# Kernel optimization log

Hardware: AMD Instinct MI355X
Metric: run time of the kernel (lower is better)

## Reference

```python
import jax, jax.numpy as jnp
import numpy as np

B = 262144
L = 16      # latent_dim
H = 64      # hidden_dim
C = 8       # num_charts
O = 32      # output_dim
TAU_MIN = 0.01
TAU_DENOM_MIN = 0.001
EPS = 0.001
LN_EPS = 1e-5


def setup_inputs() -> dict:
    key = jax.random.key(0)
    ks = jax.random.split(key, 16)
    # latents kept well inside the Poincare ball
    z_geo = 0.1 * jax.random.normal(ks[0], (B, L), dtype=jnp.float32)
    z_tex = 0.1 * jax.random.normal(ks[1], (B, L), dtype=jnp.float32)
    def lin(k, fan_in, shape):
        bound = 1.0 / np.sqrt(fan_in)
        return jax.random.uniform(k, shape, jnp.float32, -bound, bound)
    chart_w = lin(ks[2], L, (C, H, L))   # stacked per-chart Linear weights
    chart_b = lin(ks[3], L, (C, H))
    router_w = lin(ks[4], L, (C, L))
    router_b = lin(ks[5], L, (C,))
    centers = 0.02 * jax.random.normal(ks[6], (C, L), dtype=jnp.float32)
    tex_w = lin(ks[7], L, (H, L))
    tex_b = lin(ks[8], L, (H,))
    ln_g = jnp.ones((H,), jnp.float32)
    ln_b = jnp.zeros((H,), jnp.float32)
    w1 = lin(ks[9], H, (H, H))
    b1 = lin(ks[10], H, (H,))
    w2 = lin(ks[11], H, (O, H))
    b2 = lin(ks[12], H, (O,))
    return dict(z_geo=z_geo, z_tex=z_tex, chart_w=chart_w, chart_b=chart_b,
                router_w=router_w, router_b=router_b, centers=centers,
                tex_w=tex_w, tex_b=tex_b, ln_g=ln_g, ln_b=ln_b,
                w1=w1, b1=b1, w2=w2, b2=b2)


def _temperature(z):
    r2 = jnp.sum(z * z, axis=-1)                      # [B]
    denom = jnp.maximum(1.0 - r2, TAU_DENOM_MIN)
    tau = (np.sqrt(L) * denom) * 0.5
    return jnp.maximum(tau, TAU_MIN)                  # [B]


def _gelu(x):
    return jax.nn.gelu(x, approximate=False)


def reference(z_geo, z_tex, chart_w, chart_b, router_w, router_b, centers,
              tex_w, tex_b, ln_g, ln_b, w1, b1, w2, b2):
    # hyperbolic distance scores  [B, C]
    diff = z_geo[:, None, :] - centers[None, :, :]
    dist_sq = jnp.sum(diff * diff, axis=-1)
    z_sq = jnp.sum(z_geo * z_geo, axis=-1, keepdims=True)   # [B,1]
    c_sq = jnp.sum(centers * centers, axis=-1)[None, :]      # [1,C]
    denom = (1.0 - z_sq) * (1.0 - c_sq)
    arg = 1.0 + 2.0 * dist_sq / (denom + EPS)
    dist = jnp.arccosh(jnp.maximum(arg, 1.0 + EPS))
    tau = _temperature(z_geo)                                # [B]
    scores = -dist / tau[:, None]
    scores = scores + 0.1 * (z_geo @ router_w.T + router_b) / tau[:, None]
    router_weights = jax.nn.softmax(scores, axis=-1)         # [B,C]

    # dense chart projection + weighted blend
    h_stack = jnp.einsum('bl,chl->bch', z_geo, chart_w) + chart_b[None]  # [B,C,H]
    h_global = jnp.sum(h_stack * router_weights[:, :, None], axis=1)     # [B,H]
    h_tex = z_tex @ tex_w.T + tex_b
    h = h_global + h_tex

    # renderer: LayerNorm -> GELU -> Linear -> GELU -> Linear
    mu = jnp.mean(h, axis=-1, keepdims=True)
    var = jnp.mean((h - mu) ** 2, axis=-1, keepdims=True)
    hn = (h - mu) * jax.lax.rsqrt(var + LN_EPS) * ln_g + ln_b
    h1 = _gelu(_gelu(hn) @ w1.T + b1)
    x_hat = h1 @ w2.T + b2
    return x_hat, router_weights
```

## Files before the change

### kernel.cpp

```cpp
#include <hip/hip_runtime.h>
#include <hip/hip_bf16.h>
#include <hip/hip_fp16.h>


typedef __attribute__((ext_vector_type(8))) short short8;
typedef __attribute__((ext_vector_type(4))) float f32x4;

__device__ __forceinline__ int pkbf2(float a, float b) {
    union { __hip_bfloat162 h2; int i; } u;
    u.h2 = __float22bfloat162_rn(make_float2(a, b));
    return u.i;
}
__device__ __forceinline__ short pkbf1(float a) { return (short)pkbf2(a, 0.f); }

__device__ __forceinline__ float gelu_fast(float x) {
    float x2 = x * x;
    float t  = __expf(fmaf(x2, 0.07135481f, 1.5957691f) * x);
    float r  = __builtin_amdgcn_rcpf(t + 1.0f);
    return fmaf(-x, r, x);
}
__device__ __forceinline__ int bpack(int k, int n, int KT) {
    return (((n >> 4) * KT + (k >> 5)) * 64 + (n & 15) + (((k & 31) >> 3) << 4)) * 8 + (k & 7);
}
__device__ __forceinline__ int gswz(int g) {
    return g ^ (((g >> 4) & 3) << 1) ^ ((g >> 3) & 1);
}
__device__ __forceinline__ short8 packrow8(const float* base) {
    const float4* p = (const float4*)base;
    float4 a = p[0], b = p[1];
    union { short8 s; int i[4]; } f;
    f.i[0] = pkbf2(a.x, a.y); f.i[1] = pkbf2(a.z, a.w);
    f.i[2] = pkbf2(b.x, b.y); f.i[3] = pkbf2(b.z, b.w);
    return f.s;
}

__global__ void pack_weights(const float* __restrict__ cw, const float* __restrict__ cb,
                             const float* __restrict__ txw, const float* __restrict__ txb,
                             const float* __restrict__ w1,  const float* __restrict__ w2,
                             short* __restrict__ ws)
{
    const int tid = threadIdx.x;
    for (int idx = tid; idx < 160 * 64; idx += 256) {
        int k = idx >> 6, n = idx & 63;
        float v;
        if (k < 128)       v = cw[(k >> 4) * 1024 + n * 16 + (k & 15)];
        else if (k < 144)  v = txw[n * 16 + (k - 128)];
        else if (k < 152)  v = cb[(k - 144) * 64 + n];
        else if (k == 152) v = txb[n];
        else               v = 0.f;
        ws[bpack(k, n, 5)] = pkbf1(v);
    }
    for (int f = tid; f < 512; f += 256) {
        int lane = f & 63, e = f >> 6;
        int nt = e >> 1, kt = e & 1;
        int col = lane & 15, qq = lane >> 4;
        *(short8*)(ws + 10240 + f * 8) = packrow8(w1 + (nt * 16 + col) * 64 + kt * 32 + qq * 8);
    }
    {
        int f = tid;
        int lane = f & 63, e = f >> 6;
        int nt = e >> 1, kt = e & 1;
        int col = lane & 15, qq = lane >> 4;
        *(short8*)(ws + 14336 + f * 8) = packrow8(w2 + (nt * 16 + col) * 64 + kt * 32 + qq * 8);
    }
}

constexpr int SCR_OFF = 20480;
constexpr int RS_OFF  = 28672;
constexpr int SMEM_SZ = 32768;

__global__ __launch_bounds__(256, 4) void topo_mfma(
    const float* __restrict__ zg,  const float* __restrict__ ztx,
    const float* __restrict__ cw,  const float* __restrict__ cb,
    const float* __restrict__ rw,  const float* __restrict__ rb,
    const float* __restrict__ cen, const float* __restrict__ txw,
    const float* __restrict__ txb, const float* __restrict__ lng,
    const float* __restrict__ lnb, const float* __restrict__ w1,
    const float* __restrict__ b1,  const float* __restrict__ w2,
    const float* __restrict__ b2,  const short* __restrict__ wsp,
    const int prepacked,
    float* __restrict__ out, int Btot)
{
    __shared__ __align__(16) char smem[SMEM_SZ];
    short* WA = (short*)smem;
    __half* RSh = (__half*)(smem + RS_OFF);

    const int tid = threadIdx.x;
    const int wv = tid >> 6, lane = tid & 63;
    const int q = lane >> 4, col = lane & 15;
    const int sub = (lane >> 3) & 1, j = lane & 7;

    if (prepacked) {
        const int4* src = (const int4*)wsp;
        int4* dst = (int4*)smem;
        #pragma unroll
        for (int i = 0; i < 5; i++) dst[i * 256 + tid] = src[i * 256 + tid];
    } else {
        for (int idx = tid; idx < 160 * 64; idx += 256) {
            int k = idx >> 6, n = idx & 63;
            float v;
            if (k < 128)       v = cw[(k >> 4) * 1024 + n * 16 + (k & 15)];
            else if (k < 144)  v = txw[n * 16 + (k - 128)];
            else if (k < 152)  v = cb[(k - 144) * 64 + n];
            else if (k == 152) v = txb[n];
            else               v = 0.f;
            WA[bpack(k, n, 5)] = pkbf1(v);
        }
    }

    const long sG = (long)blockIdx.x * 256 + tid;
    {
        float z[16];
        const float4* pg = (const float4*)(zg + sG * 16);
        #pragma unroll
        for (int v = 0; v < 4; v++) {
            float4 a = pg[v];
            z[v*4+0]=a.x; z[v*4+1]=a.y; z[v*4+2]=a.z; z[v*4+3]=a.w;
        }
        float r2 = 0.f;
        #pragma unroll
        for (int l = 0; l < 16; l++) r2 = fmaf(z[l], z[l], r2);
        const float inv_tau = __builtin_amdgcn_rcpf(fmaxf(2.0f * fmaxf(1.0f - r2, 0.001f), 0.01f));
        const float omr2 = 1.0f - r2;
        float scv[8]; float smax = -1e30f;
        #pragma unroll
        for (int c = 0; c < 8; c++) {
            const float4* cp = (const float4*)(cen + c * 16);
            const float4* rp = (const float4*)(rw  + c * 16);
            float dsq = 0.f, csq = 0.f, dotv = 0.f;
            #pragma unroll
            for (int v = 0; v < 4; v++) {
                float4 cv = cp[v], rv = rp[v];
                float d0 = z[v*4+0] - cv.x, d1 = z[v*4+1] - cv.y;
                float d2 = z[v*4+2] - cv.z, d3 = z[v*4+3] - cv.w;
                dsq  = fmaf(d0,d0, fmaf(d1,d1, fmaf(d2,d2, fmaf(d3,d3, dsq))));
                csq  = fmaf(cv.x,cv.x, fmaf(cv.y,cv.y, fmaf(cv.z,cv.z, fmaf(cv.w,cv.w, csq))));
                dotv = fmaf(z[v*4+0],rv.x, fmaf(z[v*4+1],rv.y,
                       fmaf(z[v*4+2],rv.z, fmaf(z[v*4+3],rv.w, dotv))));
            }
            float u = 2.0f * dsq * __builtin_amdgcn_rcpf(omr2 * (1.0f - csq) + 0.001f);
            u = fmaxf(u, 0.001f);
            float dist  = __logf((1.0f + u) + __builtin_amdgcn_sqrtf(u * (u + 2.0f)));
            float score = fmaf(0.1f, dotv + rb[c], -dist) * inv_tau;
            scv[c] = score; smax = fmaxf(smax, score);
        }
        float esum = 0.f;
        #pragma unroll
        for (int c = 0; c < 8; c++) { scv[c] = __expf(scv[c] - smax); esum += scv[c]; }
        const float rinv = __builtin_amdgcn_rcpf(esum);
        union { ushort us[8]; int4 v; } hv;
        #pragma unroll
        for (int c = 0; c < 8; c++) {
            scv[c] *= rinv;
            hv.us[(c & 1) * 4 + (c >> 1)] = __half_as_ushort(__float2half_rn(scv[c]));
        }
        *(int4*)(RSh + tid * 8) = hv.v;
        float4* pr = (float4*)(out + (long)Btot * 32 + sG * 8);
        pr[0] = make_float4(scv[0], scv[1], scv[2], scv[3]);
        pr[1] = make_float4(scv[4], scv[5], scv[6], scv[7]);
    }

    short8 W1F[4][2], W2F[2][2];
    if (prepacked) {
        const short8* p1 = (const short8*)(wsp + 10240);
        #pragma unroll
        for (int nt = 0; nt < 4; nt++)
            #pragma unroll
            for (int kt = 0; kt < 2; kt++)
                W1F[nt][kt] = p1[(nt * 2 + kt) * 64 + lane];
        const short8* p2 = (const short8*)(wsp + 14336);
        #pragma unroll
        for (int nt = 0; nt < 2; nt++)
            #pragma unroll
            for (int kt = 0; kt < 2; kt++)
                W2F[nt][kt] = p2[(nt * 2 + kt) * 64 + lane];
    } else {
        const int kb = q * 8;
        #pragma unroll
        for (int nt = 0; nt < 4; nt++)
            #pragma unroll
            for (int kt = 0; kt < 2; kt++)
                W1F[nt][kt] = packrow8(w1 + (nt * 16 + col) * 64 + kt * 32 + kb);
        #pragma unroll
        for (int nt = 0; nt < 2; nt++)
            #pragma unroll
            for (int kt = 0; kt < 2; kt++)
                W2F[nt][kt] = packrow8(w2 + (nt * 16 + col) * 64 + kt * 32 + kb);
    }

    float lngv[4], lnbv[4], b1v[4], b2v[2];
    #pragma unroll
    for (int nt = 0; nt < 4; nt++) {
        lngv[nt] = lng[nt * 16 + col];
        lnbv[nt] = lnb[nt * 16 + col];
        b1v[nt]  = b1[nt * 16 + col];
    }
    b2v[0] = b2[col]; b2v[1] = b2[16 + col];

    __syncthreads();

    short* scr = (short*)(smem + SCR_OFF) + wv * 1024;
    union Frag { short8 s; int i[4]; };

    const long blockBase = (long)blockIdx.x * 256;
    const float* zrow = zg  + (blockBase + wv * 64 + col) * 16 + ((q & 1) << 3);
    const float* trow = ztx + (blockBase + wv * 64 + col) * 16 + ((q & 1) << 3);

    float4 za = ((const float4*)zrow)[0], zb = ((const float4*)zrow)[1];
    float4 ta = ((const float4*)trow)[0], tb = ((const float4*)trow)[1];

    for (int t = 0; t < 4; t++) {
        const int mBase = wv * 64 + t * 16;
        const int sL = mBase + col;
        const int rsb = sL * 8;

        float rc[4];
        {
            union { unsigned long long u; __half2 h[2]; } rr;
            rr.u = *(const unsigned long long*)(RSh + rsb + ((q >> 1) << 2));
            float2 f0 = __half22float2(rr.h[0]);
            float2 f1 = __half22float2(rr.h[1]);
            rc[0] = f0.x; rc[1] = f0.y; rc[2] = f1.x; rc[3] = f1.y;
        }

        f32x4 acc[4] = {{0.f,0.f,0.f,0.f},{0.f,0.f,0.f,0.f},{0.f,0.f,0.f,0.f},{0.f,0.f,0.f,0.f}};
        #pragma unroll
        for (int kt = 0; kt < 4; kt++) {
            float r = rc[kt];
            Frag f;
            f.i[0] = pkbf2(r * za.x, r * za.y);
            f.i[1] = pkbf2(r * za.z, r * za.w);
            f.i[2] = pkbf2(r * zb.x, r * zb.y);
            f.i[3] = pkbf2(r * zb.z, r * zb.w);
            #pragma unroll
            for (int nt = 0; nt < 4; nt++) {
                short8 bf = *(const short8*)(WA + (nt * 5 + kt) * 512 + lane * 8);
                acc[nt] = __builtin_amdgcn_mfma_f32_16x16x32_bf16(f.s, bf, acc[nt], 0, 0, 0);
            }
        }
        {
            Frag f;
            if (q < 2) {
                f.i[0] = pkbf2(ta.x, ta.y); f.i[1] = pkbf2(ta.z, ta.w);
                f.i[2] = pkbf2(tb.x, tb.y); f.i[3] = pkbf2(tb.z, tb.w);
            } else if (q == 2) {
                union { int4 u; __half2 h[4]; } rv;
                rv.u = *(const int4*)(RSh + rsb);
                float2 e0 = __half22float2(rv.h[0]);
                float2 e1 = __half22float2(rv.h[1]);
                float2 e2 = __half22float2(rv.h[2]);
                float2 e3 = __half22float2(rv.h[3]);
                f.i[0] = pkbf2(e0.x, e2.x);
                f.i[1] = pkbf2(e0.y, e2.y);
                f.i[2] = pkbf2(e1.x, e3.x);
                f.i[3] = pkbf2(e1.y, e3.y);
            } else {
                f.i[0] = pkbf2(1.0f, 0.f); f.i[1] = 0; f.i[2] = 0; f.i[3] = 0;
            }
            #pragma unroll
            for (int nt = 0; nt < 4; nt++) {
                short8 bf = *(const short8*)(WA + (nt * 5 + 4) * 512 + lane * 8);
                acc[nt] = __builtin_amdgcn_mfma_f32_16x16x32_bf16(f.s, bf, acc[nt], 0, 0, 0);
            }
        }

        if (t < 3) {
            const float4* pzn = (const float4*)(zrow + (t + 1) * 256);
            const float4* ptn = (const float4*)(trow + (t + 1) * 256);
            za = pzn[0]; zb = pzn[1]; ta = ptn[0]; tb = ptn[1];
        }

        float mu[4], rsd[4];
        #pragma unroll
        for (int reg = 0; reg < 4; reg++) {
            float a = acc[0][reg], b = acc[1][reg], c = acc[2][reg], d = acc[3][reg];
            float s  = (a + b) + (c + d);
            float s2 = fmaf(a, a, fmaf(b, b, fmaf(c, c, d * d)));
            s  += __shfl_xor(s, 1);  s  += __shfl_xor(s, 2);
            s  += __shfl_xor(s, 4);  s  += __shfl_xor(s, 8);
            s2 += __shfl_xor(s2, 1); s2 += __shfl_xor(s2, 2);
            s2 += __shfl_xor(s2, 4); s2 += __shfl_xor(s2, 8);
            float m = s * (1.0f / 64.0f);
            mu[reg]  = m;
            rsd[reg] = rsqrtf(fmaf(s2, 1.0f / 64.0f, -m * m) + 1e-5f);
        }

        #pragma unroll
        for (int nt = 0; nt < 4; nt++) {
            int high = (nt & 1) * 2 + sub;
            #pragma unroll
            for (int reg = 0; reg < 4; reg++) {
                float hn = (acc[nt][reg] - mu[reg]) * rsd[reg] * lngv[nt] + lnbv[nt];
                int grp = gswz((q * 4 + reg) + 16 * high);
                scr[(nt >> 1) * 512 + grp * 8 + j] = pkbf1(gelu_fast(hn));
            }
        }
        asm volatile("s_waitcnt lgkmcnt(0)" ::: "memory");

        short8 A2[2];
        {
            int grp = gswz(lane);
            A2[0] = *(const short8*)(scr +       grp * 8);
            A2[1] = *(const short8*)(scr + 512 + grp * 8);
        }

        #pragma unroll
        for (int nt = 0; nt < 4; nt++) {
            f32x4 a2 = {0.f, 0.f, 0.f, 0.f};
            a2 = __builtin_amdgcn_mfma_f32_16x16x32_bf16(A2[0], W1F[nt][0], a2, 0, 0, 0);
            a2 = __builtin_amdgcn_mfma_f32_16x16x32_bf16(A2[1], W1F[nt][1], a2, 0, 0, 0);
            int high = (nt & 1) * 2 + sub;
            #pragma unroll
            for (int reg = 0; reg < 4; reg++) {
                float h1v = gelu_fast(a2[reg] + b1v[nt]);
                int grp = gswz((q * 4 + reg) + 16 * high);
                scr[(nt >> 1) * 512 + grp * 8 + j] = pkbf1(h1v);
            }
        }
        asm volatile("s_waitcnt lgkmcnt(0)" ::: "memory");

        short8 A3[2];
        {
            int grp = gswz(lane);
            A3[0] = *(const short8*)(scr +       grp * 8);
            A3[1] = *(const short8*)(scr + 512 + grp * 8);
        }

        const long sOutBase = blockBase + mBase + q * 4;
        #pragma unroll
        for (int nt = 0; nt < 2; nt++) {
            f32x4 a3 = {0.f, 0.f, 0.f, 0.f};
            a3 = __builtin_amdgcn_mfma_f32_16x16x32_bf16(A3[0], W2F[nt][0], a3, 0, 0, 0);
            a3 = __builtin_amdgcn_mfma_f32_16x16x32_bf16(A3[1], W2F[nt][1], a3, 0, 0, 0);
            #pragma unroll
            for (int reg = 0; reg < 4; reg++)
                out[(sOutBase + reg) * 32 + nt * 16 + col] = a3[reg] + b2v[nt];
        }
    }
}

extern "C" void kernel_launch(void* const* d_in, const int* in_sizes, int n_in,
                              void* d_out, int out_size, void* d_ws, size_t ws_size,
                              hipStream_t stream) {
    const int B = in_sizes[0] / 16;
    const int prepacked = (d_ws != nullptr && ws_size >= 32768) ? 1 : 0;
    if (prepacked) {
        hipLaunchKernelGGL(pack_weights, dim3(1), dim3(256), 0, stream,
            (const float*)d_in[2],  (const float*)d_in[3],
            (const float*)d_in[7],  (const float*)d_in[8],
            (const float*)d_in[11], (const float*)d_in[13],
            (short*)d_ws);
    }
    dim3 grid(B / 256), block(256);
    hipLaunchKernelGGL(topo_mfma, grid, block, 0, stream,
        (const float*)d_in[0],  (const float*)d_in[1],
        (const float*)d_in[2],  (const float*)d_in[3],
        (const float*)d_in[4],  (const float*)d_in[5],
        (const float*)d_in[6],  (const float*)d_in[7],
        (const float*)d_in[8],  (const float*)d_in[9],
        (const float*)d_in[10], (const float*)d_in[11],
        (const float*)d_in[12], (const float*)d_in[13],
        (const float*)d_in[14],
        (const short*)d_ws, prepacked,
        (float*)d_out, B);
}
```

Measured before the change: 147.6 us.

## Transpose MFMA operands so activations chain through registers via lane shuffles

New measurement: 221.5 us. +50.1%, slower.

```diff
diff --git a/kernel.cpp b/kernel.cpp
--- a/kernel.cpp
+++ b/kernel.cpp
@@ -18,12 +18,6 @@
     float t  = __expf(fmaf(x2, 0.07135481f, 1.5957691f) * x);
     float r  = __builtin_amdgcn_rcpf(t + 1.0f);
     return fmaf(-x, r, x);
-}
-__device__ __forceinline__ int bpack(int k, int n, int KT) {
-    return (((n >> 4) * KT + (k >> 5)) * 64 + (n & 15) + (((k & 31) >> 3) << 4)) * 8 + (k & 7);
-}
-__device__ __forceinline__ int gswz(int g) {
-    return g ^ (((g >> 4) & 3) << 1) ^ ((g >> 3) & 1);
 }
 __device__ __forceinline__ short8 packrow8(const float* base) {
     const float4* p = (const float4*)base;
@@ -34,40 +28,73 @@
     return f.s;
 }
 
+__device__ __forceinline__ void bfly(int (&D)[4][2], bool hi32, bool hi16) {
+    #pragma unroll
+    for (int n1 = 0; n1 < 2; n1++)
+        #pragma unroll
+        for (int s = 0; s < 2; s++) {
+            int d0 = D[n1*2+0][s], d1 = D[n1*2+1][s];
+            int send = hi32 ? d0 : d1;
+            int recv = __shfl_xor(send, 32);
+            D[n1*2+0][s] = hi32 ? recv : d0;
+            D[n1*2+1][s] = hi32 ? d1 : recv;
+        }
+    #pragma unroll
+    for (int n1 = 0; n1 < 2; n1++)
+        #pragma unroll
+        for (int s = 0; s < 2; s++) {
+            int d0 = D[n1*2+0][s], d1 = D[n1*2+1][s];
+            int send = hi16 ? d0 : d1;
+            int recv = __shfl_xor(send, 16);
+            D[n1*2+0][s] = hi16 ? recv : d0;
+            D[n1*2+1][s] = hi16 ? d1 : recv;
+        }
+}
+
 __global__ void pack_weights(const float* __restrict__ cw, const float* __restrict__ cb,
                              const float* __restrict__ txw, const float* __restrict__ txb,
                              const float* __restrict__ w1,  const float* __restrict__ w2,
+                             const float* __restrict__ cen, const float* __restrict__ rb,
                              short* __restrict__ ws)
 {
     const int tid = threadIdx.x;
-    for (int idx = tid; idx < 160 * 64; idx += 256) {
-        int k = idx >> 6, n = idx & 63;
+    for (int idx = tid; idx < 10240; idx += 256) {
+        int j = idx & 7, lane = (idx >> 3) & 63, g = idx >> 9;
+        int nt = g / 5, kt = g - nt * 5;
+        int k = kt * 32 + (lane >> 4) * 8 + j;
+        int n = nt * 16 + (lane & 15);
         float v;
         if (k < 128)       v = cw[(k >> 4) * 1024 + n * 16 + (k & 15)];
         else if (k < 144)  v = txw[n * 16 + (k - 128)];
         else if (k < 152)  v = cb[(k - 144) * 64 + n];
         else if (k == 152) v = txb[n];
         else               v = 0.f;
-        ws[bpack(k, n, 5)] = pkbf1(v);
-    }
-    for (int f = tid; f < 512; f += 256) {
+        ws[idx] = pkbf1(v);
+    }
+    for (int f = tid; f < 768; f += 256) {
         int lane = f & 63, e = f >> 6;
-        int nt = e >> 1, kt = e & 1;
         int col = lane & 15, qq = lane >> 4;
-        *(short8*)(ws + 10240 + f * 8) = packrow8(w1 + (nt * 16 + col) * 64 + kt * 32 + qq * 8);
-    }
-    {
-        int f = tid;
-        int lane = f & 63, e = f >> 6;
-        int nt = e >> 1, kt = e & 1;
-        int col = lane & 15, qq = lane >> 4;
-        *(short8*)(ws + 14336 + f * 8) = packrow8(w2 + (nt * 16 + col) * 64 + kt * 32 + qq * 8);
-    }
-}
-
-constexpr int SCR_OFF = 20480;
-constexpr int RS_OFF  = 28672;
-constexpr int SMEM_SZ = 32768;
+        if (e < 8) {
+            int nt = e >> 1, kt = e & 1;
+            *(short8*)(ws + 10240 + f * 8) =
+                packrow8(w1 + (nt * 16 + col) * 64 + kt * 32 + qq * 8);
+        } else {
+            int e2 = e - 8, nt = e2 >> 1, kt = e2 & 1;
+            *(short8*)(ws + 14336 + (e2 * 64 + lane) * 8) =
+                packrow8(w2 + (nt * 16 + col) * 64 + kt * 32 + qq * 8);
+        }
+    }
+    if (tid < 8) {
+        float csq = 0.f;
+        for (int l = 0; l < 16; l++) { float cv = cen[tid * 16 + l]; csq = fmaf(cv, cv, csq); }
+        ((float4*)((char*)ws + 32768))[tid] = make_float4(csq, 1.0f - csq, 0.1f * rb[tid], 0.f);
+    }
+}
+
+constexpr int W1L_OFF = 20480;
+constexpr int W2L_OFF = 28672;
+constexpr int RS_OFF  = 32768;
+constexpr int SMEM_SZ = 36864;
 
 __global__ __launch_bounds__(256, 4) void topo_mfma(
     const float* __restrict__ zg,  const float* __restrict__ ztx,
@@ -82,29 +109,47 @@
     float* __restrict__ out, int Btot)
 {
     __shared__ __align__(16) char smem[SMEM_SZ];
-    short* WA = (short*)smem;
+    short* WAF = (short*)smem;
+    const short8* W1L = (const short8*)(smem + W1L_OFF);
+    const short8* W2L = (const short8*)(smem + W2L_OFF);
     __half* RSh = (__half*)(smem + RS_OFF);
 
     const int tid = threadIdx.x;
     const int wv = tid >> 6, lane = tid & 63;
     const int q = lane >> 4, col = lane & 15;
-    const int sub = (lane >> 3) & 1, j = lane & 7;
+    const bool hi32 = (lane & 32) != 0, hi16 = (lane & 16) != 0;
 
     if (prepacked) {
         const int4* src = (const int4*)wsp;
         int4* dst = (int4*)smem;
         #pragma unroll
-        for (int i = 0; i < 5; i++) dst[i * 256 + tid] = src[i * 256 + tid];
+        for (int i = 0; i < 8; i++) dst[i * 256 + tid] = src[i * 256 + tid];
     } else {
-        for (int idx = tid; idx < 160 * 64; idx += 256) {
-            int k = idx >> 6, n = idx & 63;
+        for (int idx = tid; idx < 10240; idx += 256) {
+            int j = idx & 7, ln = (idx >> 3) & 63, g = idx >> 9;
+            int nt = g / 5, kt = g - nt * 5;
+            int k = kt * 32 + (ln >> 4) * 8 + j;
+            int n = nt * 16 + (ln & 15);
             float v;
             if (k < 128)       v = cw[(k >> 4) * 1024 + n * 16 + (k & 15)];
             else if (k < 144)  v = txw[n * 16 + (k - 128)];
             else if (k < 152)  v = cb[(k - 144) * 64 + n];
             else if (k == 152) v = txb[n];
             else               v = 0.f;
-            WA[bpack(k, n, 5)] = pkbf1(v);
+            WAF[idx] = pkbf1(v);
+        }
+        for (int f = tid; f < 768; f += 256) {
+            int ln = f & 63, e = f >> 6;
+            int c_ = ln & 15, qq = ln >> 4;
+            if (e < 8) {
+                int nt = e >> 1, kt = e & 1;
+                *(short8*)(smem + W1L_OFF + f * 16) =
+                    packrow8(w1 + (nt * 16 + c_) * 64 + kt * 32 + qq * 8);
+            } else {
+                int e2 = e - 8, nt = e2 >> 1, kt = e2 & 1;
+                *(short8*)(smem + W2L_OFF + (e2 * 64 + ln) * 16) =
+                    packrow8(w2 + (nt * 16 + c_) * 64 + kt * 32 + qq * 8);
+            }
         }
     }
 
@@ -122,26 +167,35 @@
         for (int l = 0; l < 16; l++) r2 = fmaf(z[l], z[l], r2);
         const float inv_tau = __builtin_amdgcn_rcpf(fmaxf(2.0f * fmaxf(1.0f - r2, 0.001f), 0.01f));
         const float omr2 = 1.0f - r2;
+        const float4* cvp = (const float4*)((const char*)wsp + 32768);
         float scv[8]; float smax = -1e30f;
         #pragma unroll
         for (int c = 0; c < 8; c++) {
+            float csq, omc2, rb1;
+            if (prepacked) {
+                float4 kv = cvp[c]; csq = kv.x; omc2 = kv.y; rb1 = kv.z;
+            } else {
+                csq = 0.f;
+                #pragma unroll
+                for (int l = 0; l < 16; l++) { float cv = cen[c*16+l]; csq = fmaf(cv, cv, csq); }
+                omc2 = 1.0f - csq; rb1 = 0.1f * rb[c];
+            }
             const float4* cp = (const float4*)(cen + c * 16);
             const float4* rp = (const float4*)(rw  + c * 16);
-            float dsq = 0.f, csq = 0.f, dotv = 0.f;
+            float zc = 0.f, dotv = 0.f;
             #pragma unroll
             for (int v = 0; v < 4; v++) {
                 float4 cv = cp[v], rv = rp[v];
-                float d0 = z[v*4+0] - cv.x, d1 = z[v*4+1] - cv.y;
-                float d2 = z[v*4+2] - cv.z, d3 = z[v*4+3] - cv.w;
-                dsq  = fmaf(d0,d0, fmaf(d1,d1, fmaf(d2,d2, fmaf(d3,d3, dsq))));
-                csq  = fmaf(cv.x,cv.x, fmaf(cv.y,cv.y, fmaf(cv.z,cv.z, fmaf(cv.w,cv.w, csq))));
+                zc   = fmaf(z[v*4+0],cv.x, fmaf(z[v*4+1],cv.y,
+                       fmaf(z[v*4+2],cv.z, fmaf(z[v*4+3],cv.w, zc))));
                 dotv = fmaf(z[v*4+0],rv.x, fmaf(z[v*4+1],rv.y,
                        fmaf(z[v*4+2],rv.z, fmaf(z[v*4+3],rv.w, dotv))));
             }
-            float u = 2.0f * dsq * __builtin_amdgcn_rcpf(omr2 * (1.0f - csq) + 0.001f);
+            float dsq = fmaf(-2.0f, zc, r2 + csq);
+            float u = 2.0f * dsq * __builtin_amdgcn_rcpf(omr2 * omc2 + 0.001f);
             u = fmaxf(u, 0.001f);
             float dist  = __logf((1.0f + u) + __builtin_amdgcn_sqrtf(u * (u + 2.0f)));
-            float score = fmaf(0.1f, dotv + rb[c], -dist) * inv_tau;
+            float score = (fmaf(0.1f, dotv, rb1) - dist) * inv_tau;
             scv[c] = score; smax = fmaxf(smax, score);
         }
         float esum = 0.f;
@@ -160,47 +214,21 @@
         pr[1] = make_float4(scv[4], scv[5], scv[6], scv[7]);
     }
 
-    short8 W1F[4][2], W2F[2][2];
-    if (prepacked) {
-        const short8* p1 = (const short8*)(wsp + 10240);
-        #pragma unroll
-        for (int nt = 0; nt < 4; nt++)
-            #pragma unroll
-            for (int kt = 0; kt < 2; kt++)
-                W1F[nt][kt] = p1[(nt * 2 + kt) * 64 + lane];
-        const short8* p2 = (const short8*)(wsp + 14336);
-        #pragma unroll
-        for (int nt = 0; nt < 2; nt++)
-            #pragma unroll
-            for (int kt = 0; kt < 2; kt++)
-                W2F[nt][kt] = p2[(nt * 2 + kt) * 64 + lane];
-    } else {
-        const int kb = q * 8;
-        #pragma unroll
-        for (int nt = 0; nt < 4; nt++)
-            #pragma unroll
-            for (int kt = 0; kt < 2; kt++)
-                W1F[nt][kt] = packrow8(w1 + (nt * 16 + col) * 64 + kt * 32 + kb);
-        #pragma unroll
-        for (int nt = 0; nt < 2; nt++)
-            #pragma unroll
-            for (int kt = 0; kt < 2; kt++)
-                W2F[nt][kt] = packrow8(w2 + (nt * 16 + col) * 64 + kt * 32 + kb);
-    }
-
-    float lngv[4], lnbv[4], b1v[4], b2v[2];
+    float lngv[4][4], lnbv[4][4], b1v[4][4], b2v[2];
     #pragma unroll
     for (int nt = 0; nt < 4; nt++) {
-        lngv[nt] = lng[nt * 16 + col];
-        lnbv[nt] = lnb[nt * 16 + col];
-        b1v[nt]  = b1[nt * 16 + col];
+        float4 g4 = *(const float4*)(lng + nt * 16 + q * 4);
+        float4 bb = *(const float4*)(lnb + nt * 16 + q * 4);
+        float4 o4 = *(const float4*)(b1  + nt * 16 + q * 4);
+        lngv[nt][0]=g4.x; lngv[nt][1]=g4.y; lngv[nt][2]=g4.z; lngv[nt][3]=g4.w;
+        lnbv[nt][0]=bb.x; lnbv[nt][1]=bb.y; lnbv[nt][2]=bb.z; lnbv[nt][3]=bb.w;
+        b1v [nt][0]=o4.x; b1v [nt][1]=o4.y; b1v [nt][2]=o4.z; b1v [nt][3]=o4.w;
     }
     b2v[0] = b2[col]; b2v[1] = b2[16 + col];
 
     __syncthreads();
 
-    short* scr = (short*)(smem + SCR_OFF) + wv * 1024;
-    union Frag { short8 s; int i[4]; };
+    union FragU { short8 s; int i[4]; };
 
     const long blockBase = (long)blockIdx.x * 256;
     const float* zrow = zg  + (blockBase + wv * 64 + col) * 16 + ((q & 1) << 3);
@@ -227,19 +255,19 @@
         #pragma unroll
         for (int kt = 0; kt < 4; kt++) {
             float r = rc[kt];
-            Frag f;
+            FragU f;
             f.i[0] = pkbf2(r * za.x, r * za.y);
             f.i[1] = pkbf2(r * za.z, r * za.w);
             f.i[2] = pkbf2(r * zb.x, r * zb.y);
             f.i[3] = pkbf2(r * zb.z, r * zb.w);
             #pragma unroll
             for (int nt = 0; nt < 4; nt++) {
-                short8 bf = *(const short8*)(WA + (nt * 5 + kt) * 512 + lane * 8);
-                acc[nt] = __builtin_amdgcn_mfma_f32_16x16x32_bf16(f.s, bf, acc[nt], 0, 0, 0);
+                short8 wa = *(const short8*)(WAF + ((nt * 5 + kt) * 64 + lane) * 8);
+                acc[nt] = __builtin_amdgcn_mfma_f32_16x16x32_bf16(wa, f.s, acc[nt], 0, 0, 0);
             }
         }
         {
-            Frag f;
+            FragU f;
             if (q < 2) {
                 f.i[0] = pkbf2(ta.x, ta.y); f.i[1] = pkbf2(ta.z, ta.w);
                 f.i[2] = pkbf2(tb.x, tb.y); f.i[3] = pkbf2(tb.z, tb.w);
@@ -259,8 +287,8 @@
             }
             #pragma unroll
             for (int nt = 0; nt < 4; nt++) {
-                short8 bf = *(const short8*)(WA + (nt * 5 + 4) * 512 + lane * 8);
-                acc[nt] = __builtin_amdgcn_mfma_f32_16x16x32_bf16(f.s, bf, acc[nt], 0, 0, 0);
+                short8 wa = *(const short8*)(WAF + ((nt * 5 + 4) * 64 + lane) * 8);
+                acc[nt] = __builtin_amdgcn_mfma_f32_16x16x32_bf16(wa, f.s, acc[nt], 0, 0, 0);
             }
         }
 
@@ -270,68 +298,61 @@
             za = pzn[0]; zb = pzn[1]; ta = ptn[0]; tb = ptn[1];
         }
 
-        float mu[4], rsd[4];
-        #pragma unroll
-        for (int reg = 0; reg < 4; reg++) {
-            float a = acc[0][reg], b = acc[1][reg], c = acc[2][reg], d = acc[3][reg];
-            float s  = (a + b) + (c + d);
-            float s2 = fmaf(a, a, fmaf(b, b, fmaf(c, c, d * d)));
-            s  += __shfl_xor(s, 1);  s  += __shfl_xor(s, 2);
-            s  += __shfl_xor(s, 4);  s  += __shfl_xor(s, 8);
-            s2 += __shfl_xor(s2, 1); s2 += __shfl_xor(s2, 2);
-            s2 += __shfl_xor(s2, 4); s2 += __shfl_xor(s2, 8);
-            float m = s * (1.0f / 64.0f);
-            mu[reg]  = m;
-            rsd[reg] = rsqrtf(fmaf(s2, 1.0f / 64.0f, -m * m) + 1e-5f);
-        }
-
-        #pragma unroll
-        for (int nt = 0; nt < 4; nt++) {
-            int high = (nt & 1) * 2 + sub;
+        float s = 0.f, s2 = 0.f;
+        #pragma unroll
+        for (int nt = 0; nt < 4; nt++)
             #pragma unroll
             for (int reg = 0; reg < 4; reg++) {
-                float hn = (acc[nt][reg] - mu[reg]) * rsd[reg] * lngv[nt] + lnbv[nt];
-                int grp = gswz((q * 4 + reg) + 16 * high);
-                scr[(nt >> 1) * 512 + grp * 8 + j] = pkbf1(gelu_fast(hn));
-            }
-        }
-        asm volatile("s_waitcnt lgkmcnt(0)" ::: "memory");
-
-        short8 A2[2];
-        {
-            int grp = gswz(lane);
-            A2[0] = *(const short8*)(scr +       grp * 8);
-            A2[1] = *(const short8*)(scr + 512 + grp * 8);
-        }
-
+                float v = acc[nt][reg];
+                s += v; s2 = fmaf(v, v, s2);
+            }
+        s  += __shfl_xor(s, 16);  s  += __shfl_xor(s, 32);
+        s2 += __shfl_xor(s2, 16); s2 += __shfl_xor(s2, 32);
+        float mu  = s * (1.0f / 64.0f);
+        float rsd = rsqrtf(fmaf(s2, 1.0f / 64.0f, -mu * mu) + 1e-5f);
+
+        int D[4][2];
+        #pragma unroll
+        for (int nt = 0; nt < 4; nt++)
+            #pragma unroll
+            for (int sx = 0; sx < 2; sx++) {
+                float g0 = gelu_fast(fmaf((acc[nt][2*sx  ] - mu) * rsd, lngv[nt][2*sx  ], lnbv[nt][2*sx  ]));
+                float g1 = gelu_fast(fmaf((acc[nt][2*sx+1] - mu) * rsd, lngv[nt][2*sx+1], lnbv[nt][2*sx+1]));
+                D[nt][sx] = pkbf2(g0, g1);
+            }
+        bfly(D, hi32, hi16);
+        FragU Gf0, Gf1;
+        Gf0.i[0]=D[0][0]; Gf0.i[1]=D[0][1]; Gf0.i[2]=D[1][0]; Gf0.i[3]=D[1][1];
+        Gf1.i[0]=D[2][0]; Gf1.i[1]=D[2][1]; Gf1.i[2]=D[3][0]; Gf1.i[3]=D[3][1];
+
+        int D2[4][2];
         #pragma unroll
         for (int nt = 0; nt < 4; nt++) {
             f32x4 a2 = {0.f, 0.f, 0.f, 0.f};
-            a2 = __builtin_amdgcn_mfma_f32_16x16x32_bf16(A2[0], W1F[nt][0], a2, 0, 0, 0);
-            a2 = __builtin_amdgcn_mfma_f32_16x16x32_bf16(A2[1], W1F[nt][1], a2, 0, 0, 0);
-            int high = (nt & 1) * 2 + sub;
-            #pragma unroll
-            for (int reg = 0; reg < 4; reg++) {
-                float h1v = gelu_fast(a2[reg] + b1v[nt]);
-                int grp = gswz((q * 4 + reg) + 16 * high);
-                scr[(nt >> 1) * 512 + grp * 8 + j] = pkbf1(h1v);
-            }
-        }
-        asm volatile("s_waitcnt lgkmcnt(0)" ::: "memory");
-
-        short8 A3[2];
-        {
-            int grp = gswz(lane);
-            A3[0] = *(const short8*)(scr +       grp * 8);
-            A3[1] = *(const short8*)(scr + 512 + grp * 8);
-        }
+            short8 wA = W1L[(nt * 2 + 0) * 64 + lane];
+            short8 wB = W1L[(nt * 2 + 1) * 64 + lane];
+            a2 = __builtin_amdgcn_mfma_f32_16x16x32_bf16(wA, Gf0.s, a2, 0, 0, 0);
+            a2 = __builtin_amdgcn_mfma_f32_16x16x32_bf16(wB, Gf1.s, a2, 0, 0, 0);
+            #pragma unroll
+            for (int sx = 0; sx < 2; sx++) {
+                float h0 = gelu_fast(a2[2*sx  ] + b1v[nt][2*sx  ]);
+                float h1 = gelu_fast(a2[2*sx+1] + b1v[nt][2*sx+1]);
+                D2[nt][sx] = pkbf2(h0, h1);
+            }
+        }
+        bfly(D2, hi32, hi16);
+        FragU A3f0, A3f1;
+        A3f0.i[0]=D2[0][0]; A3f0.i[1]=D2[0][1]; A3f0.i[2]=D2[1][0]; A3f0.i[3]=D2[1][1];
+        A3f1.i[0]=D2[2][0]; A3f1.i[1]=D2[2][1]; A3f1.i[2]=D2[3][0]; A3f1.i[3]=D2[3][1];
 
         const long sOutBase = blockBase + mBase + q * 4;
         #pragma unroll
         for (int nt = 0; nt < 2; nt++) {
             f32x4 a3 = {0.f, 0.f, 0.f, 0.f};
-            a3 = __builtin_amdgcn_mfma_f32_16x16x32_bf16(A3[0], W2F[nt][0], a3, 0, 0, 0);
-            a3 = __builtin_amdgcn_mfma_f32_16x16x32_bf16(A3[1], W2F[nt][1], a3, 0, 0, 0);
+            short8 wA = W2L[(nt * 2 + 0) * 64 + lane];
+            short8 wB = W2L[(nt * 2 + 1) * 64 + lane];
+            a3 = __builtin_amdgcn_mfma_f32_16x16x32_bf16(A3f0.s, wA, a3, 0, 0, 0);
+            a3 = __builtin_amdgcn_mfma_f32_16x16x32_bf16(A3f1.s, wB, a3, 0, 0, 0);
             #pragma unroll
             for (int reg = 0; reg < 4; reg++)
                 out[(sOutBase + reg) * 32 + nt * 16 + col] = a3[reg] + b2v[nt];
@@ -343,12 +364,13 @@
                               void* d_out, int out_size, void* d_ws, size_t ws_size,
                               hipStream_t stream) {
     const int B = in_sizes[0] / 16;
-    const int prepacked = (d_ws != nullptr && ws_size >= 32768) ? 1 : 0;
+    const int prepacked = (d_ws != nullptr && ws_size >= 32896) ? 1 : 0;
     if (prepacked) {
         hipLaunchKernelGGL(pack_weights, dim3(1), dim3(256), 0, stream,
             (const float*)d_in[2],  (const float*)d_in[3],
             (const float*)d_in[7],  (const float*)d_in[8],
             (const float*)d_in[11], (const float*)d_in[13],
+            (const float*)d_in[6],  (const float*)d_in[5],
             (short*)d_ws);
     }
     dim3 grid(B / 256), block(256);
```

## Move W2 fragments to LDS, precompute center norms, restructure first MFMA loop

Applied to the files above, without the earlier changes.

New measurement: 151.9 us. 1.03x slower.

```diff
diff --git a/kernel.cpp b/kernel.cpp
--- a/kernel.cpp
+++ b/kernel.cpp
@@ -37,6 +37,7 @@
 __global__ void pack_weights(const float* __restrict__ cw, const float* __restrict__ cb,
                              const float* __restrict__ txw, const float* __restrict__ txb,
                              const float* __restrict__ w1,  const float* __restrict__ w2,
+                             const float* __restrict__ cen, const float* __restrict__ rb,
                              short* __restrict__ ws)
 {
     const int tid = threadIdx.x;
@@ -63,11 +64,17 @@
         int col = lane & 15, qq = lane >> 4;
         *(short8*)(ws + 14336 + f * 8) = packrow8(w2 + (nt * 16 + col) * 64 + kt * 32 + qq * 8);
     }
+    if (tid < 8) {
+        float csq = 0.f;
+        for (int l = 0; l < 16; l++) { float cv = cen[tid * 16 + l]; csq = fmaf(cv, cv, csq); }
+        ((float4*)((char*)ws + 32768))[tid] = make_float4(csq, 1.0f - csq, 0.1f * rb[tid], 0.f);
+    }
 }
 
 constexpr int SCR_OFF = 20480;
 constexpr int RS_OFF  = 28672;
-constexpr int SMEM_SZ = 32768;
+constexpr int W2L_OFF = 32768;
+constexpr int SMEM_SZ = 36864;
 
 __global__ __launch_bounds__(256, 4) void topo_mfma(
     const float* __restrict__ zg,  const float* __restrict__ ztx,
@@ -84,6 +91,7 @@
     __shared__ __align__(16) char smem[SMEM_SZ];
     short* WA = (short*)smem;
     __half* RSh = (__half*)(smem + RS_OFF);
+    const short8* W2L = (const short8*)(smem + W2L_OFF);
 
     const int tid = threadIdx.x;
     const int wv = tid >> 6, lane = tid & 63;
@@ -95,6 +103,7 @@
         int4* dst = (int4*)smem;
         #pragma unroll
         for (int i = 0; i < 5; i++) dst[i * 256 + tid] = src[i * 256 + tid];
+        ((int4*)(smem + W2L_OFF))[tid] = ((const int4*)((const char*)wsp + 28672))[tid];
     } else {
         for (int idx = tid; idx < 160 * 64; idx += 256) {
             int k = idx >> 6, n = idx & 63;
@@ -106,6 +115,12 @@
             else               v = 0.f;
             WA[bpack(k, n, 5)] = pkbf1(v);
         }
+        {
+            int e = tid >> 6, ln = tid & 63;
+            int nt = e >> 1, kt = e & 1;
+            *(short8*)(smem + W2L_OFF + (e * 64 + ln) * 16) =
+                packrow8(w2 + (nt * 16 + (ln & 15)) * 64 + kt * 32 + (ln >> 4) * 8);
+        }
     }
 
     const long sG = (long)blockIdx.x * 256 + tid;
@@ -122,26 +137,35 @@
         for (int l = 0; l < 16; l++) r2 = fmaf(z[l], z[l], r2);
         const float inv_tau = __builtin_amdgcn_rcpf(fmaxf(2.0f * fmaxf(1.0f - r2, 0.001f), 0.01f));
         const float omr2 = 1.0f - r2;
+        const float4* cvp = (const float4*)((const char*)wsp + 32768);
         float scv[8]; float smax = -1e30f;
         #pragma unroll
         for (int c = 0; c < 8; c++) {
+            float csq, omc2, rb1;
+            if (prepacked) {
+                float4 kv = cvp[c]; csq = kv.x; omc2 = kv.y; rb1 = kv.z;
+            } else {
+                csq = 0.f;
+                #pragma unroll
+                for (int l = 0; l < 16; l++) { float cv = cen[c*16+l]; csq = fmaf(cv, cv, csq); }
+                omc2 = 1.0f - csq; rb1 = 0.1f * rb[c];
+            }
             const float4* cp = (const float4*)(cen + c * 16);
             const float4* rp = (const float4*)(rw  + c * 16);
-            float dsq = 0.f, csq = 0.f, dotv = 0.f;
+            float zc = 0.f, dotv = 0.f;
             #pragma unroll
             for (int v = 0; v < 4; v++) {
                 float4 cv = cp[v], rv = rp[v];
-                float d0 = z[v*4+0] - cv.x, d1 = z[v*4+1] - cv.y;
-                float d2 = z[v*4+2] - cv.z, d3 = z[v*4+3] - cv.w;
-                dsq  = fmaf(d0,d0, fmaf(d1,d1, fmaf(d2,d2, fmaf(d3,d3, dsq))));
-                csq  = fmaf(cv.x,cv.x, fmaf(cv.y,cv.y, fmaf(cv.z,cv.z, fmaf(cv.w,cv.w, csq))));
+                zc   = fmaf(z[v*4+0],cv.x, fmaf(z[v*4+1],cv.y,
+                       fmaf(z[v*4+2],cv.z, fmaf(z[v*4+3],cv.w, zc))));
                 dotv = fmaf(z[v*4+0],rv.x, fmaf(z[v*4+1],rv.y,
                        fmaf(z[v*4+2],rv.z, fmaf(z[v*4+3],rv.w, dotv))));
             }
-            float u = 2.0f * dsq * __builtin_amdgcn_rcpf(omr2 * (1.0f - csq) + 0.001f);
+            float dsq = fmaf(-2.0f, zc, r2 + csq);
+            float u = 2.0f * dsq * __builtin_amdgcn_rcpf(omr2 * omc2 + 0.001f);
             u = fmaxf(u, 0.001f);
             float dist  = __logf((1.0f + u) + __builtin_amdgcn_sqrtf(u * (u + 2.0f)));
-            float score = fmaf(0.1f, dotv + rb[c], -dist) * inv_tau;
+            float score = (fmaf(0.1f, dotv, rb1) - dist) * inv_tau;
             scv[c] = score; smax = fmaxf(smax, score);
         }
         float esum = 0.f;
@@ -160,7 +184,7 @@
         pr[1] = make_float4(scv[4], scv[5], scv[6], scv[7]);
     }
 
-    short8 W1F[4][2], W2F[2][2];
+    short8 W1F[4][2];
     if (prepacked) {
         const short8* p1 = (const short8*)(wsp + 10240);
         #pragma unroll
@@ -168,12 +192,6 @@
             #pragma unroll
             for (int kt = 0; kt < 2; kt++)
                 W1F[nt][kt] = p1[(nt * 2 + kt) * 64 + lane];
-        const short8* p2 = (const short8*)(wsp + 14336);
-        #pragma unroll
-        for (int nt = 0; nt < 2; nt++)
-            #pragma unroll
-            for (int kt = 0; kt < 2; kt++)
-                W2F[nt][kt] = p2[(nt * 2 + kt) * 64 + lane];
     } else {
         const int kb = q * 8;
         #pragma unroll
@@ -181,13 +199,7 @@
             #pragma unroll
             for (int kt = 0; kt < 2; kt++)
                 W1F[nt][kt] = packrow8(w1 + (nt * 16 + col) * 64 + kt * 32 + kb);
-        #pragma unroll
-        for (int nt = 0; nt < 2; nt++)
-            #pragma unroll
-            for (int kt = 0; kt < 2; kt++)
-                W2F[nt][kt] = packrow8(w2 + (nt * 16 + col) * 64 + kt * 32 + kb);
-    }
-
+    }
     float lngv[4], lnbv[4], b1v[4], b2v[2];
     #pragma unroll
     for (int nt = 0; nt < 4; nt++) {
@@ -210,9 +222,9 @@
     float4 ta = ((const float4*)trow)[0], tb = ((const float4*)trow)[1];
 
     for (int t = 0; t < 4; t++) {
-        const int mBase = wv * 64 + t * 16;
-        const int sL = mBase + col;
-        const int rsb = sL * 8;
+        const int  mBase = wv * 64 + t * 16;
+        const int  sL = mBase + col;
+        const int  rsb = sL * 8;
 
         float rc[4];
         {
@@ -223,7 +235,7 @@
             rc[0] = f0.x; rc[1] = f0.y; rc[2] = f1.x; rc[3] = f1.y;
         }
 
-        f32x4 acc[4] = {{0.f,0.f,0.f,0.f},{0.f,0.f,0.f,0.f},{0.f,0.f,0.f,0.f},{0.f,0.f,0.f,0.f}};
+        short8 A1[5];
         #pragma unroll
         for (int kt = 0; kt < 4; kt++) {
             float r = rc[kt];
@@ -232,11 +244,7 @@
             f.i[1] = pkbf2(r * za.z, r * za.w);
             f.i[2] = pkbf2(r * zb.x, r * zb.y);
             f.i[3] = pkbf2(r * zb.z, r * zb.w);
-            #pragma unroll
-            for (int nt = 0; nt < 4; nt++) {
-                short8 bf = *(const short8*)(WA + (nt * 5 + kt) * 512 + lane * 8);
-                acc[nt] = __builtin_amdgcn_mfma_f32_16x16x32_bf16(f.s, bf, acc[nt], 0, 0, 0);
-            }
+            A1[kt] = f.s;
         }
         {
             Frag f;
@@ -257,11 +265,20 @@
             } else {
                 f.i[0] = pkbf2(1.0f, 0.f); f.i[1] = 0; f.i[2] = 0; f.i[3] = 0;
             }
-            #pragma unroll
-            for (int nt = 0; nt < 4; nt++) {
-                short8 bf = *(const short8*)(WA + (nt * 5 + 4) * 512 + lane * 8);
-                acc[nt] = __builtin_amdgcn_mfma_f32_16x16x32_bf16(f.s, bf, acc[nt], 0, 0, 0);
-            }
+            A1[4] = f.s;
+        }
+
+        float h[4][4];
+        #pragma unroll
+        for (int nt = 0; nt < 4; nt++) {
+            f32x4 acc = {0.f, 0.f, 0.f, 0.f};
+            #pragma unroll
+            for (int kt = 0; kt < 5; kt++) {
+                short8 bf = *(const short8*)(WA + (nt * 5 + kt) * 512 + lane * 8);
+                acc = __builtin_amdgcn_mfma_f32_16x16x32_bf16(A1[kt], bf, acc, 0, 0, 0);
+            }
+            #pragma unroll
+            for (int reg = 0; reg < 4; reg++) h[nt][reg] = acc[reg];
         }
 
         if (t < 3) {
@@ -273,7 +290,7 @@
         float mu[4], rsd[4];
         #pragma unroll
         for (int reg = 0; reg < 4; reg++) {
-            float a = acc[0][reg], b = acc[1][reg], c = acc[2][reg], d = acc[3][reg];
+            float a = h[0][reg], b = h[1][reg], c = h[2][reg], d = h[3][reg];
             float s  = (a + b) + (c + d);
             float s2 = fmaf(a, a, fmaf(b, b, fmaf(c, c, d * d)));
             s  += __shfl_xor(s, 1);  s  += __shfl_xor(s, 2);
@@ -290,7 +307,7 @@
             int high = (nt & 1) * 2 + sub;
             #pragma unroll
             for (int reg = 0; reg < 4; reg++) {
-                float hn = (acc[nt][reg] - mu[reg]) * rsd[reg] * lngv[nt] + lnbv[nt];
+                float hn = (h[nt][reg] - mu[reg]) * rsd[reg] * lngv[nt] + lnbv[nt];
                 int grp = gswz((q * 4 + reg) + 16 * high);
                 scr[(nt >> 1) * 512 + grp * 8 + j] = pkbf1(gelu_fast(hn));
             }
@@ -306,13 +323,13 @@
 
         #pragma unroll
         for (int nt = 0; nt < 4; nt++) {
-            f32x4 a2 = {0.f, 0.f, 0.f, 0.f};
-            a2 = __builtin_amdgcn_mfma_f32_16x16x32_bf16(A2[0], W1F[nt][0], a2, 0, 0, 0);
-            a2 = __builtin_amdgcn_mfma_f32_16x16x32_bf16(A2[1], W1F[nt][1], a2, 0, 0, 0);
+            f32x4 acc = {0.f, 0.f, 0.f, 0.f};
+            acc = __builtin_amdgcn_mfma_f32_16x16x32_bf16(A2[0], W1F[nt][0], acc, 0, 0, 0);
+            acc = __builtin_amdgcn_mfma_f32_16x16x32_bf16(A2[1], W1F[nt][1], acc, 0, 0, 0);
             int high = (nt & 1) * 2 + sub;
             #pragma unroll
             for (int reg = 0; reg < 4; reg++) {
-                float h1v = gelu_fast(a2[reg] + b1v[nt]);
+                float h1v = gelu_fast(acc[reg] + b1v[nt]);
                 int grp = gswz((q * 4 + reg) + 16 * high);
                 scr[(nt >> 1) * 512 + grp * 8 + j] = pkbf1(h1v);
             }
@@ -329,12 +346,14 @@
         const long sOutBase = blockBase + mBase + q * 4;
         #pragma unroll
         for (int nt = 0; nt < 2; nt++) {
-            f32x4 a3 = {0.f, 0.f, 0.f, 0.f};
-            a3 = __builtin_amdgcn_mfma_f32_16x16x32_bf16(A3[0], W2F[nt][0], a3, 0, 0, 0);
-            a3 = __builtin_amdgcn_mfma_f32_16x16x32_bf16(A3[1], W2F[nt][1], a3, 0, 0, 0);
+            f32x4 acc = {0.f, 0.f, 0.f, 0.f};
+            short8 wA = W2L[(nt * 2 + 0) * 64 + lane];
+            short8 wB = W2L[(nt * 2 + 1) * 64 + lane];
+            acc = __builtin_amdgcn_mfma_f32_16x16x32_bf16(A3[0], wA, acc, 0, 0, 0);
+            acc = __builtin_amdgcn_mfma_f32_16x16x32_bf16(A3[1], wB, acc, 0, 0, 0);
             #pragma unroll
             for (int reg = 0; reg < 4; reg++)
-                out[(sOutBase + reg) * 32 + nt * 16 + col] = a3[reg] + b2v[nt];
+                out[(sOutBase + reg) * 32 + nt * 16 + col] = acc[reg] + b2v[nt];
         }
     }
 }
@@ -343,12 +362,13 @@
                               void* d_out, int out_size, void* d_ws, size_t ws_size,
                               hipStream_t stream) {
     const int B = in_sizes[0] / 16;
-    const int prepacked = (d_ws != nullptr && ws_size >= 32768) ? 1 : 0;
+    const int prepacked = (d_ws != nullptr && ws_size >= 32896) ? 1 : 0;
     if (prepacked) {
         hipLaunchKernelGGL(pack_weights, dim3(1), dim3(256), 0, stream,
             (const float*)d_in[2],  (const float*)d_in[3],
             (const float*)d_in[7],  (const float*)d_in[8],
             (const float*)d_in[11], (const float*)d_in[13],
+            (const float*)d_in[6],  (const float*)d_in[5],
             (short*)d_ws);
     }
     dim3 grid(B / 256), block(256);
```
